# Optimization experiments

Measured on AMD Instinct MI355X. Metric: run time of the kernel, lower is better.

Reference implementation:

```python
import math
import jax, jax.numpy as jnp
import numpy as np

B, N, T, C, H = 16, 307, 24, 128, 8
D = C // H
FACTOR = 5
S = min(FACTOR * int(np.ceil(np.log(T))), T)   # sample_k (U_part) = 20
U = S                                          # n_top u = 20


def _pos_emb(t_len, c):
    pos = jnp.arange(t_len, dtype=jnp.float32)[:, None]
    div = jnp.exp(jnp.arange(0, c, 2, dtype=jnp.float32) * (-math.log(10000.0) / c))
    pe = jnp.zeros((t_len, c), dtype=jnp.float32)
    pe = pe.at[:, 0::2].set(jnp.sin(pos * div))
    pe = pe.at[:, 1::2].set(jnp.cos(pos * div))
    return pe  # [T, C]


def _layernorm(x, g, b, eps=1e-5):
    m = x.mean(-1, keepdims=True)
    v = ((x - m) ** 2).mean(-1, keepdims=True)
    return (x - m) / jnp.sqrt(v + eps) * g + b


def _forward(query, time_encoder, index_sample,
             emb_minute, emb_hour, emb_weekday, emb_month, emb_year,
             Wq, Wk, Wv, Wo, bo, ff_w1, ff_b1, ff_w2, ff_b2,
             ln1_g, ln1_b, ln2_g, ln2_b):
    # DataEmbedding: x + positional + temporal (dropout = identity in eval)
    pe = _pos_emb(T, C)                                   # [T, C]
    te = (emb_minute[time_encoder[..., 0]] + emb_hour[time_encoder[..., 1]]
          + emb_weekday[time_encoder[..., 2]] + emb_month[time_encoder[..., 3]]
          + emb_year[time_encoder[..., 4]])               # [B, T, C]
    x = query + pe[None, None, :, :] + te[:, None, :, :]  # [B, N, T, C]

    # QKV projections -> [B, H, N, T, D]
    def proj(inp, W):
        return (inp @ W).reshape(B, N, T, H, D).transpose(0, 3, 1, 2, 4)
    Q, K, V = proj(x, Wq), proj(x, Wk), proj(x, Wv)

    # ProbSparse: sample S keys per query position
    K_samp = K[:, :, :, index_sample, :]                  # [B, H, N, T, S, D]
    QK_samp = jnp.einsum('bhntd,bhntsd->bhnts', Q, K_samp)
    M = QK_samp.max(-1) - QK_samp.sum(-1) / S             # [B, H, N, T]
    _, M_top = jax.lax.top_k(M, U)                        # [B, H, N, U]

    Q_red = jnp.take_along_axis(Q, M_top[..., None], axis=3)  # [B, H, N, U, D]
    scores = jnp.einsum('bhnud,bhntd->bhnut', Q_red, K) * (1.0 / math.sqrt(D))
    attn = jax.nn.softmax(scores, axis=-1)
    upd = jnp.einsum('bhnut,bhntd->bhnud', attn, V)       # [B, H, N, U, D]

    # initial context = mean over T, then scatter-update top-u query rows
    ctx = jnp.broadcast_to(V.mean(axis=3, keepdims=True), V.shape)
    ctx = ctx.at[jnp.arange(B)[:, None, None, None],
                 jnp.arange(H)[None, :, None, None],
                 jnp.arange(N)[None, None, :, None],
                 M_top].set(upd)

    ctx = ctx.transpose(0, 2, 3, 1, 4).reshape(B, N, T, C)
    att_out = ctx @ Wo + bo

    x1 = _layernorm(att_out + x, ln1_g, ln1_b)
    ff = jax.nn.relu(x1 @ ff_w1 + ff_b1) @ ff_w2 + ff_b2
    out = _layernorm(ff + x1, ln2_g, ln2_b)
    return out


def setup_inputs() -> dict:
    key = jax.random.key(0)
    ks = jax.random.split(key, 32)
    def nrm(i, shape, s=0.02):
        return jax.random.normal(ks[i], shape, dtype=jnp.float32) * s
    inp = {
        'value': jax.random.normal(ks[0], (B, N, T, C), dtype=jnp.float32),
        'key_in': jax.random.normal(ks[1], (B, N, T, C), dtype=jnp.float32),
        'query': jax.random.normal(ks[2], (B, N, T, C), dtype=jnp.float32),
        't': 1,
        'time_encoder': jax.random.randint(ks[3], (B, T, 5), 0, 10),
        'index_sample': jax.random.randint(ks[4], (T, S), 0, T),
        'emb_minute': nrm(5, (70, C), 1.0), 'emb_hour': nrm(6, (30, C), 1.0),
        'emb_weekday': nrm(7, (10, C), 1.0), 'emb_month': nrm(8, (40, C), 1.0),
        'emb_year': nrm(9, (400, C), 1.0),
        'Wq': nrm(10, (C, C)), 'Wk': nrm(11, (C, C)), 'Wv': nrm(12, (C, C)),
        'Wo': nrm(13, (C, C)), 'bo': jnp.zeros((C,), jnp.float32),
        'ff_w1': nrm(14, (C, 4 * C)), 'ff_b1': jnp.zeros((4 * C,), jnp.float32),
        'ff_w2': nrm(15, (4 * C, C)), 'ff_b2': jnp.zeros((C,), jnp.float32),
        'ln1_g': jnp.ones((C,), jnp.float32), 'ln1_b': jnp.zeros((C,), jnp.float32),
        'ln2_g': jnp.ones((C,), jnp.float32), 'ln2_b': jnp.zeros((C,), jnp.float32),
    }
    return inp


def reference(value, key_in, query, t, time_encoder, index_sample,
              emb_minute, emb_hour, emb_weekday, emb_month, emb_year,
              Wq, Wk, Wv, Wo, bo, ff_w1, ff_b1, ff_w2, ff_b2,
              ln1_g, ln1_b, ln2_g, ln2_b):
    # value, key_in, t are accepted but unused, matching the torch module
    return _forward(query, time_encoder, index_sample,
                    emb_minute, emb_hour, emb_weekday, emb_month, emb_year,
                    Wq, Wk, Wv, Wo, bo, ff_w1, ff_b1, ff_w2, ff_b2,
                    ln1_g, ln1_b, ln2_g, ln2_b)
```

## Files before the change

### kernel.cpp

```cpp
#include <hip/hip_runtime.h>
#include <hip/hip_bf16.h>
#include <cmath>

namespace {
constexpr int B_ = 16, N_ = 307, T_ = 24, C_ = 128, H_ = 8, D_ = 16, S_ = 20, U_ = 20;
constexpr int NROW = B_ * N_ * T_;
constexpr int NX = NROW * C_;
constexpr int TEPE_N = B_ * T_ * C_;
constexpr int FF = 4 * C_;
constexpr int BM = 32;
constexpr int NBLK_MM = NROW / BM;
constexpr int BMT = 64;
constexpr int NBLK_T = NROW / BMT;
constexpr int NUNIT = B_ * H_ * N_;
}

typedef __attribute__((ext_vector_type(8))) short short8;
typedef __attribute__((ext_vector_type(4))) short short4_;
typedef __attribute__((ext_vector_type(4))) float f32x4;

__device__ inline short f2bf(float v) {
    union { float f; unsigned u; } a; a.f = v;
    unsigned r = a.u + 0x7fff + ((a.u >> 16) & 1);
    return (short)(r >> 16);
}
__device__ inline float bf2f(short s) {
    return __bfloat162float(*(const __hip_bfloat16*)&s);
}

__global__ void k_tepe(const int* __restrict__ te,
                       const float* __restrict__ e_min, const float* __restrict__ e_hr,
                       const float* __restrict__ e_wd, const float* __restrict__ e_mo,
                       const float* __restrict__ e_yr, float* __restrict__ tepe,
                       const int* __restrict__ idxs, unsigned char* __restrict__ cntg) {
    int i = blockIdx.x * blockDim.x + threadIdx.x;
    if (i < TEPE_N) {
        int c = i & (C_ - 1);
        int bt = i >> 7;
        int t = bt % T_;
        const int* enc = te + bt * 5;
        float v = e_min[enc[0] * C_ + c] + e_hr[enc[1] * C_ + c] + e_wd[enc[2] * C_ + c]
                + e_mo[enc[3] * C_ + c] + e_yr[enc[4] * C_ + c];
        float ang = (float)t * expf(-(float)(c & ~1) * (9.210340371976184f / 128.0f));
        v += (c & 1) ? cosf(ang) : sinf(ang);
        tepe[i] = v;
    }
    if (blockIdx.x == 0) {
        __shared__ int scnt[T_ * 32];
        for (int j = threadIdx.x; j < T_ * 32; j += 256) scnt[j] = 0;
        __syncthreads();
        for (int j = threadIdx.x; j < T_ * S_; j += 256) {
            int t = j / S_;
            atomicAdd(&scnt[t * 32 + idxs[j]], 1);
        }
        __syncthreads();
        for (int j = threadIdx.x; j < 192; j += 256) {
            unsigned v = (unsigned)scnt[4 * j] | ((unsigned)scnt[4 * j + 1] << 8)
                       | ((unsigned)scnt[4 * j + 2] << 16) | ((unsigned)scnt[4 * j + 3] << 24);
            ((unsigned*)cntg)[j] = v;
        }
    }
}

__global__ void k_wcvt_qkv(const float* __restrict__ Wq, const float* __restrict__ Wk,
                           const float* __restrict__ Wv, short* __restrict__ wqkvf) {
    int i = blockIdx.x * 256 + threadIdx.x;
    int tile = i >> 9, l = (i >> 3) & 63, e = i & 7;
    int c_tile = tile >> 2, ks = tile & 3;
    int c_all = c_tile * 16 + (l & 15);
    int k = ks * 32 + (l >> 4) * 8 + e;
    int m = c_all >> 7, c = c_all & (C_ - 1);
    const float* W = (m == 0) ? Wq : (m == 1) ? Wk : Wv;
    wqkvf[i] = f2bf(W[k * C_ + c]);
}

__global__ void k_wcvt2(const float* __restrict__ w1, const float* __restrict__ w2,
                        const float* __restrict__ Wo,
                        short* __restrict__ w1f, short* __restrict__ w2f,
                        short* __restrict__ wof) {
    int i = blockIdx.x * 256 + threadIdx.x;
    if (i < C_ * FF) {
        int tile = i >> 9, l = (i >> 3) & 63, e = i & 7;
        int jtile = tile >> 2, ks = tile & 3;
        int j = jtile * 16 + (l & 15);
        int k = ks * 32 + (l >> 4) * 8 + e;
        w1f[i] = f2bf(w1[k * FF + j]);
    } else if (i < 2 * C_ * FF) {
        int i2 = i - C_ * FF;
        int tile = i2 >> 9, l = (i2 >> 3) & 63, e = i2 & 7;
        int c_tile = tile >> 4, ks = tile & 15;
        int c = c_tile * 16 + (l & 15);
        int j = ks * 32 + (l >> 4) * 8 + e;
        w2f[i2] = f2bf(w2[j * C_ + c]);
    } else {
        int i3 = i - 2 * C_ * FF;
        int tile = i3 >> 9, l = (i3 >> 3) & 63, e = i3 & 7;
        int c_tile = tile >> 2, ks = tile & 3;
        int c = c_tile * 16 + (l & 15);
        int k = ks * 32 + (l >> 4) * 8 + e;
        wof[i3] = f2bf(Wo[k * C_ + c]);
    }
}

__global__ __launch_bounds__(256) void k_qkv_mfma(
    const float* __restrict__ query, const float* __restrict__ tepe,
    const short* __restrict__ wqkvf,
    short* __restrict__ Q, short* __restrict__ K, short* __restrict__ V) {
    __shared__ __align__(16) short xs[BM * C_];
    int tid = threadIdx.x;
    int r0 = blockIdx.x * BM;
    {
        int row = tid >> 3;
        int cb = (tid & 7) * 16;
        int gr = r0 + row;
        int t = gr % T_;
        int b = gr / (N_ * T_);
        const float* qsrc = query + (size_t)gr * C_ + cb;
        const float* tsrc = tepe + (size_t)(b * T_ + t) * C_ + cb;
        int swz0 = (row & 7) << 3;
#pragma unroll
        for (int i = 0; i < 4; i++) {
            float4 q4 = *(const float4*)(qsrc + 4 * i);
            float4 t4 = *(const float4*)(tsrc + 4 * i);
            short4_ sv;
            sv.x = f2bf(q4.x + t4.x); sv.y = f2bf(q4.y + t4.y);
            sv.z = f2bf(q4.z + t4.z); sv.w = f2bf(q4.w + t4.w);
            *(short4_*)&xs[(row * C_ + cb + 4 * i) ^ swz0] = sv;
        }
    }
    __syncthreads();
    int w = tid >> 6, l = tid & 63;
    int lr = l & 15, lk = l >> 4;
    int swz = (lr & 7) << 3;
    short8 bx[2][4];
#pragma unroll
    for (int rt = 0; rt < 2; rt++)
#pragma unroll
        for (int ks = 0; ks < 4; ks++)
            bx[rt][ks] = *(const short8*)&xs[((rt * 16 + lr) * C_ + ks * 32 + lk * 8) ^ swz];
    size_t base[2];
#pragma unroll
    for (int rt = 0; rt < 2; rt++) {
        int gr = r0 + rt * 16 + lr;
        int t = gr % T_;
        int n = (gr / T_) % N_;
        int b = gr / (N_ * T_);
        base[rt] = ((size_t)b * H_ * N_ + n) * (T_ * D_) + t * D_;
    }
#pragma unroll
    for (int jt = 0; jt < 6; jt++) {
        int ctile = w * 6 + jt;
        const short* ap = wqkvf + (size_t)ctile * 2048 + l * 8;
        short8 acur[4];
#pragma unroll
        for (int ks = 0; ks < 4; ks++) acur[ks] = *(const short8*)(ap + ks * 512);
        f32x4 acc[2] = {{0.f, 0.f, 0.f, 0.f}, {0.f, 0.f, 0.f, 0.f}};
#pragma unroll
        for (int ks = 0; ks < 4; ks++) {
#pragma unroll
            for (int rt = 0; rt < 2; rt++)
                acc[rt] = __builtin_amdgcn_mfma_f32_16x16x32_bf16(acur[ks], bx[rt][ks], acc[rt], 0, 0, 0);
        }
        int c0 = ctile * 16 + lk * 4;
        int m = c0 >> 7;
        int c = c0 & (C_ - 1);
        int h = c >> 4, d = c & 15;
        short* dst = (m == 0) ? Q : (m == 1) ? K : V;
#pragma unroll
        for (int rt = 0; rt < 2; rt++) {
            short4_ sv;
            sv.x = f2bf(acc[rt][0]); sv.y = f2bf(acc[rt][1]);
            sv.z = f2bf(acc[rt][2]); sv.w = f2bf(acc[rt][3]);
            *(short4_*)&dst[base[rt] + (size_t)h * (N_ * T_ * D_) + d] = sv;
        }
    }
}

__global__ __launch_bounds__(256) void k_attn(
    const short* __restrict__ Q, const short* __restrict__ K, const short* __restrict__ V,
    const unsigned char* __restrict__ cntg, short* __restrict__ ctx) {
    __shared__ __align__(16) short Qbf[4][32 * 24], Kbf[4][32 * 24];
    __shared__ __align__(16) short Vt[4][16 * 40];
    __shared__ __align__(16) short Pbf[4][32 * 40];
    __shared__ unsigned char cntS[T_ * 32];
    __shared__ float Mv[4][T_];
    __shared__ int keepS[4][T_];
    __shared__ float meanVs[4][D_];
    int tid = threadIdx.x;
    int wid = tid >> 6, l = tid & 63;
    int e = blockIdx.x * 4 + wid;
    const short* qb = Q + (size_t)e * (T_ * D_);
    const short* kb = K + (size_t)e * (T_ * D_);
    const short* vb = V + (size_t)e * (T_ * D_);
    if (l < 48) {
        int t = l >> 1, hf = l & 1;
        *(short8*)&Qbf[wid][t * 24 + hf * 8] = *(const short8*)(qb + t * 16 + hf * 8);
        *(short8*)&Kbf[wid][t * 24 + hf * 8] = *(const short8*)(kb + t * 16 + hf * 8);
    }
    for (int i = l; i < 96; i += 64) {
        int t = i >> 2, c4 = i & 3;
        short4_ v = *(const short4_*)(vb + t * 16 + c4 * 4);
        Vt[wid][(c4 * 4 + 0) * 40 + t] = v.x;
        Vt[wid][(c4 * 4 + 1) * 40 + t] = v.y;
        Vt[wid][(c4 * 4 + 2) * 40 + t] = v.z;
        Vt[wid][(c4 * 4 + 3) * 40 + t] = v.w;
    }
    for (int i = l; i < 128; i += 64) {
        int d = i >> 3, c = 24 + (i & 7);
        Vt[wid][d * 40 + c] = 0;
    }
    if (tid < 192) ((int*)cntS)[tid] = ((const int*)cntg)[tid];
    __syncthreads();
    if (l >= 48) {
        int d = l - 48;
        float s = 0.f;
        for (int t = 0; t < T_; t++) s += bf2f(Vt[wid][d * 40 + t]);
        meanVs[wid][d] = s * (1.0f / T_);
    }
    int lr = l & 15, lk = l >> 4;
    short8 zz = {};
    short8 kf0 = zz, kf1 = zz, qf0 = zz, qf1 = zz;
    if (lk < 2) {
        kf0 = *(const short8*)&Kbf[wid][lr * 24 + lk * 8];
        kf1 = *(const short8*)&Kbf[wid][(16 + lr) * 24 + lk * 8];
        qf0 = *(const short8*)&Qbf[wid][lr * 24 + lk * 8];
        qf1 = *(const short8*)&Qbf[wid][(16 + lr) * 24 + lk * 8];
    }
    f32x4 zf = {0.f, 0.f, 0.f, 0.f};
    f32x4 s00 = __builtin_amdgcn_mfma_f32_16x16x32_bf16(kf0, qf0, zf, 0, 0, 0);
    f32x4 s01 = __builtin_amdgcn_mfma_f32_16x16x32_bf16(kf1, qf0, zf, 0, 0, 0);
    f32x4 s10 = __builtin_amdgcn_mfma_f32_16x16x32_bf16(kf0, qf1, zf, 0, 0, 0);
    f32x4 s11 = __builtin_amdgcn_mfma_f32_16x16x32_bf16(kf1, qf1, zf, 0, 0, 0);
#pragma unroll
    for (int rt = 0; rt < 2; rt++) {
        int t = rt * 16 + lr;
        int tt = (t < T_) ? t : 0;
        f32x4 c0 = rt ? s10 : s00;
        f32x4 c1 = rt ? s11 : s01;
        float mx = -1e30f, sm = 0.f;
#pragma unroll
        for (int i = 0; i < 4; i++) {
            int cA = cntS[tt * 32 + lk * 4 + i];
            if (cA) { mx = fmaxf(mx, c0[i]); sm += (float)cA * c0[i]; }
        }
        if (lk < 2) {
#pragma unroll
            for (int i = 0; i < 4; i++) {
                int cB = cntS[tt * 32 + 16 + lk * 4 + i];
                if (cB) { mx = fmaxf(mx, c1[i]); sm += (float)cB * c1[i]; }
            }
        }
        mx = fmaxf(mx, __shfl_xor(mx, 16));
        mx = fmaxf(mx, __shfl_xor(mx, 32));
        sm += __shfl_xor(sm, 16);
        sm += __shfl_xor(sm, 32);
        if (lk == 0 && t < T_) Mv[wid][t] = mx - sm * (1.0f / S_);
    }
    __syncthreads();
    if (l < T_) {
        float mt = Mv[wid][l];
        int cnt2 = 0;
        for (int t2 = 0; t2 < T_; t2++) {
            float m2 = Mv[wid][t2];
            cnt2 += (m2 > mt) || (m2 == mt && t2 < l);
        }
        keepS[wid][l] = (cnt2 < U_) ? 1 : 0;
    }
#pragma unroll
    for (int rt = 0; rt < 2; rt++) {
        f32x4 c0 = rt ? s10 : s00;
        f32x4 c1 = rt ? s11 : s01;
        float lm = fmaxf(fmaxf(c0[0], c0[1]), fmaxf(c0[2], c0[3]));
        if (lk < 2) lm = fmaxf(lm, fmaxf(fmaxf(c1[0], c1[1]), fmaxf(c1[2], c1[3])));
        lm = fmaxf(lm, __shfl_xor(lm, 16));
        lm = fmaxf(lm, __shfl_xor(lm, 32));
        float e0[4], e1[4];
        float ls = 0.f;
#pragma unroll
        for (int i = 0; i < 4; i++) { e0[i] = __expf(0.25f * (c0[i] - lm)); ls += e0[i]; }
#pragma unroll
        for (int i = 0; i < 4; i++) { e1[i] = (lk < 2) ? __expf(0.25f * (c1[i] - lm)) : 0.f; ls += e1[i]; }
        ls += __shfl_xor(ls, 16);
        ls += __shfl_xor(ls, 32);
        float inv = 1.0f / ls;
        short4_ w0, w1;
        w0.x = f2bf(e0[0] * inv); w0.y = f2bf(e0[1] * inv);
        w0.z = f2bf(e0[2] * inv); w0.w = f2bf(e0[3] * inv);
        w1.x = f2bf(e1[0] * inv); w1.y = f2bf(e1[1] * inv);
        w1.z = f2bf(e1[2] * inv); w1.w = f2bf(e1[3] * inv);
        int trow = rt * 16 + lr;
        *(short4_*)&Pbf[wid][trow * 40 + lk * 4] = w0;
        *(short4_*)&Pbf[wid][trow * 40 + 16 + lk * 4] = w1;
    }
    __syncthreads();
    short8 vf = *(const short8*)&Vt[wid][lr * 40 + lk * 8];
    short8 pf0 = *(const short8*)&Pbf[wid][lr * 40 + lk * 8];
    short8 pf1 = *(const short8*)&Pbf[wid][(16 + lr) * 40 + lk * 8];
    f32x4 u0 = __builtin_amdgcn_mfma_f32_16x16x32_bf16(vf, pf0, zf, 0, 0, 0);
    f32x4 u1 = __builtin_amdgcn_mfma_f32_16x16x32_bf16(vf, pf1, zf, 0, 0, 0);
    int b = e / (H_ * N_);
    int h = (e / N_) % H_;
    int n = e % N_;
    float4 mv4 = *(const float4*)&meanVs[wid][lk * 4];
#pragma unroll
    for (int rt = 0; rt < 2; rt++) {
        int t = rt * 16 + lr;
        if (t < T_) {
            f32x4 u = rt ? u1 : u0;
            float4 o;
            if (keepS[wid][t]) { o.x = u[0]; o.y = u[1]; o.z = u[2]; o.w = u[3]; }
            else o = mv4;
            short4_ sv;
            sv.x = f2bf(o.x); sv.y = f2bf(o.y); sv.z = f2bf(o.z); sv.w = f2bf(o.w);
            *(short4_*)&ctx[((size_t)(b * N_ + n) * T_ + t) * C_ + h * D_ + lk * 4] = sv;
        }
    }
}

__global__ __launch_bounds__(256, 4) void k_tail(
    const short* __restrict__ ctx, const short* __restrict__ wof, const float* __restrict__ bo,
    const float* __restrict__ query, const float* __restrict__ tepe,
    const float* __restrict__ g1, const float* __restrict__ b1,
    const short* __restrict__ w1f, const float* __restrict__ b1f,
    const short* __restrict__ w2f, const float* __restrict__ b2f,
    const float* __restrict__ g2, const float* __restrict__ b2ln,
    float* __restrict__ out) {
    __shared__ __align__(16) char smem[81920];
    short* hbf = (short*)smem;
    float (*yf)[132] = (float(*)[132])smem;
    short* x1bf = (short*)(smem + 65536);
    int tid = threadIdx.x;
    int r0 = blockIdx.x * BMT;
    int w = tid >> 6, l = tid & 63;
    int lr = l & 15, lk = l >> 4;
    int swz = (lr & 7) << 3;
    int myloc = w * 16 + lr;
    int gr = r0 + myloc;
    int t = gr % T_;
    int b = gr / (N_ * T_);
    const short* csrc = ctx + (size_t)gr * C_;
    short8 bc[4];
#pragma unroll
    for (int ks = 0; ks < 4; ks++)
        bc[ks] = *(const short8*)(csrc + ks * 32 + lk * 8);
    const float* qsrc = query + (size_t)gr * C_;
    const float* tsrc = tepe + (size_t)(b * T_ + t) * C_;
    float4 xres[8];
#pragma unroll
    for (int ct = 0; ct < 8; ct++) {
        float4 q4 = *(const float4*)(qsrc + ct * 16 + lk * 4);
        float4 t4 = *(const float4*)(tsrc + ct * 16 + lk * 4);
        xres[ct].x = q4.x + t4.x; xres[ct].y = q4.y + t4.y;
        xres[ct].z = q4.z + t4.z; xres[ct].w = q4.w + t4.w;
    }
#pragma unroll
    for (int ct = 0; ct < 8; ct++) {
        f32x4 acc = {0.f, 0.f, 0.f, 0.f};
#pragma unroll
        for (int ks = 0; ks < 4; ks++) {
            short8 aw = *(const short8*)(wof + (size_t)(ct * 4 + ks) * 512 + l * 8);
            acc = __builtin_amdgcn_mfma_f32_16x16x32_bf16(aw, bc[ks], acc, 0, 0, 0);
        }
        float4 bo4 = *(const float4*)(bo + ct * 16 + lk * 4);
        xres[ct].x += acc[0] + bo4.x;
        xres[ct].y += acc[1] + bo4.y;
        xres[ct].z += acc[2] + bo4.z;
        xres[ct].w += acc[3] + bo4.w;
    }
    {
        float s = 0.f;
#pragma unroll
        for (int ct = 0; ct < 8; ct++)
            s += xres[ct].x + xres[ct].y + xres[ct].z + xres[ct].w;
        s += __shfl_xor(s, 16);
        s += __shfl_xor(s, 32);
        float mean = s * (1.f / C_);
        float vv = 0.f;
#pragma unroll
        for (int ct = 0; ct < 8; ct++) {
            float dx = xres[ct].x - mean, dy = xres[ct].y - mean;
            float dz = xres[ct].z - mean, dw = xres[ct].w - mean;
            vv += dx * dx + dy * dy + dz * dz + dw * dw;
        }
        vv += __shfl_xor(vv, 16);
        vv += __shfl_xor(vv, 32);
        float rstd = rsqrtf(vv * (1.f / C_) + 1e-5f);
#pragma unroll
        for (int ct = 0; ct < 8; ct++) {
            float4 gv = *(const float4*)(g1 + ct * 16 + lk * 4);
            float4 bv = *(const float4*)(b1 + ct * 16 + lk * 4);
            short4_ xv;
            xv.x = f2bf((xres[ct].x - mean) * rstd * gv.x + bv.x);
            xv.y = f2bf((xres[ct].y - mean) * rstd * gv.y + bv.y);
            xv.z = f2bf((xres[ct].z - mean) * rstd * gv.z + bv.z);
            xv.w = f2bf((xres[ct].w - mean) * rstd * gv.w + bv.w);
            *(short4_*)&x1bf[(myloc * C_ + ct * 16 + lk * 4) ^ swz] = xv;
        }
    }
    const short* w1base = w1f + (size_t)(w * 8) * 2048 + l * 8;
    short8 acur[4];
#pragma unroll
    for (int ks = 0; ks < 4; ks++) acur[ks] = *(const short8*)(w1base + ks * 512);
    __syncthreads();
    {
        short8 bx[4][4];
#pragma unroll
        for (int rt = 0; rt < 4; rt++)
#pragma unroll
            for (int ks = 0; ks < 4; ks++)
                bx[rt][ks] = *(const short8*)&x1bf[((rt * 16 + lr) * C_ + ks * 32 + lk * 8) ^ swz];
#pragma unroll
        for (int jt = 0; jt < 8; jt++) {
            short8 anxt[4];
            if (jt < 7) {
#pragma unroll
                for (int ks = 0; ks < 4; ks++)
                    anxt[ks] = *(const short8*)(w1base + (size_t)(jt + 1) * 2048 + ks * 512);
            }
            f32x4 a1[4] = {{0.f, 0.f, 0.f, 0.f}, {0.f, 0.f, 0.f, 0.f},
                           {0.f, 0.f, 0.f, 0.f}, {0.f, 0.f, 0.f, 0.f}};
#pragma unroll
            for (int ks = 0; ks < 4; ks++) {
#pragma unroll
                for (int rt = 0; rt < 4; rt++)
                    a1[rt] = __builtin_amdgcn_mfma_f32_16x16x32_bf16(acur[ks], bx[rt][ks], a1[rt], 0, 0, 0);
            }
            int j0 = (w * 8 + jt) * 16 + lk * 4;
            float4 b1v = *(const float4*)(b1f + j0);
#pragma unroll
            for (int rt = 0; rt < 4; rt++) {
                int rr = rt * 16 + lr;
                short4_ hv;
                hv.x = f2bf(fmaxf(a1[rt][0] + b1v.x, 0.f));
                hv.y = f2bf(fmaxf(a1[rt][1] + b1v.y, 0.f));
                hv.z = f2bf(fmaxf(a1[rt][2] + b1v.z, 0.f));
                hv.w = f2bf(fmaxf(a1[rt][3] + b1v.w, 0.f));
                *(short4_*)&hbf[(rr * FF + j0) ^ swz] = hv;
            }
#pragma unroll
            for (int ks = 0; ks < 4; ks++) acur[ks] = anxt[ks];
        }
    }
    short8 aA[2];
#pragma unroll
    for (int ct = 0; ct < 2; ct++)
        aA[ct] = *(const short8*)(w2f + (size_t)((w * 2 + ct) * 16) * 512 + l * 8);
    __syncthreads();
    f32x4 acc2[2][4] = {{{0.f, 0.f, 0.f, 0.f}, {0.f, 0.f, 0.f, 0.f},
                         {0.f, 0.f, 0.f, 0.f}, {0.f, 0.f, 0.f, 0.f}},
                        {{0.f, 0.f, 0.f, 0.f}, {0.f, 0.f, 0.f, 0.f},
                         {0.f, 0.f, 0.f, 0.f}, {0.f, 0.f, 0.f, 0.f}}};
#pragma unroll 4
    for (int ks = 0; ks < 16; ks++) {
        short8 aB[2];
        if (ks < 15) {
#pragma unroll
            for (int ct = 0; ct < 2; ct++)
                aB[ct] = *(const short8*)(w2f + (size_t)((w * 2 + ct) * 16 + ks + 1) * 512 + l * 8);
        }
        short8 hx[4];
#pragma unroll
        for (int rt = 0; rt < 4; rt++)
            hx[rt] = *(const short8*)&hbf[((rt * 16 + lr) * FF + ks * 32 + lk * 8) ^ swz];
#pragma unroll
        for (int ct = 0; ct < 2; ct++)
#pragma unroll
            for (int rt = 0; rt < 4; rt++)
                acc2[ct][rt] = __builtin_amdgcn_mfma_f32_16x16x32_bf16(aA[ct], hx[rt], acc2[ct][rt], 0, 0, 0);
#pragma unroll
        for (int ct = 0; ct < 2; ct++) aA[ct] = aB[ct];
    }
    float4 res[2][4], b2v[2];
#pragma unroll
    for (int ct = 0; ct < 2; ct++) {
        int cc = (w * 2 + ct) * 16 + lk * 4;
        b2v[ct] = *(const float4*)(b2f + cc);
#pragma unroll
        for (int rt = 0; rt < 4; rt++) {
            short4_ rb = *(const short4_*)&x1bf[((rt * 16 + lr) * C_ + cc) ^ swz];
            res[ct][rt].x = bf2f(rb.x); res[ct][rt].y = bf2f(rb.y);
            res[ct][rt].z = bf2f(rb.z); res[ct][rt].w = bf2f(rb.w);
        }
    }
    __syncthreads();
#pragma unroll
    for (int ct = 0; ct < 2; ct++) {
        int cc = (w * 2 + ct) * 16 + lk * 4;
#pragma unroll
        for (int rt = 0; rt < 4; rt++) {
            int rr = rt * 16 + lr;
            float4 o;
            o.x = acc2[ct][rt][0] + b2v[ct].x + res[ct][rt].x;
            o.y = acc2[ct][rt][1] + b2v[ct].y + res[ct][rt].y;
            o.z = acc2[ct][rt][2] + b2v[ct].z + res[ct][rt].z;
            o.w = acc2[ct][rt][3] + b2v[ct].w + res[ct][rt].w;
            *(float4*)&yf[rr][cc] = o;
        }
    }
    __syncthreads();
#pragma unroll
    for (int half = 0; half < 2; half++) {
        int r = (tid >> 3) + half * 32;
        int q = tid & 7;
        int cb = q * 16;
        float vals[16];
        float s = 0.f;
#pragma unroll
        for (int i = 0; i < 16; i++) { vals[i] = yf[r][cb + i]; s += vals[i]; }
        s += __shfl_xor(s, 1, 8);
        s += __shfl_xor(s, 2, 8);
        s += __shfl_xor(s, 4, 8);
        float mean = s * (1.f / C_);
        float vv = 0.f;
#pragma unroll
        for (int i = 0; i < 16; i++) { float d = vals[i] - mean; vv += d * d; }
        vv += __shfl_xor(vv, 1, 8);
        vv += __shfl_xor(vv, 2, 8);
        vv += __shfl_xor(vv, 4, 8);
        float rstd = rsqrtf(vv * (1.f / C_) + 1e-5f);
        float* op = out + (size_t)(r0 + r) * C_ + cb;
#pragma unroll
        for (int i4 = 0; i4 < 4; i4++) {
            float4 gv = *(const float4*)(g2 + cb + 4 * i4);
            float4 bv = *(const float4*)(b2ln + cb + 4 * i4);
            float4 ov;
            ov.x = (vals[4 * i4 + 0] - mean) * rstd * gv.x + bv.x;
            ov.y = (vals[4 * i4 + 1] - mean) * rstd * gv.y + bv.y;
            ov.z = (vals[4 * i4 + 2] - mean) * rstd * gv.z + bv.z;
            ov.w = (vals[4 * i4 + 3] - mean) * rstd * gv.w + bv.w;
            *(float4*)(op + 4 * i4) = ov;
        }
    }
}

extern "C" void kernel_launch(void* const* d_in, const int* in_sizes, int n_in,
                              void* d_out, int out_size, void* d_ws, size_t ws_size,
                              hipStream_t stream) {
    const float* query = (const float*)d_in[2];
    const int* time_enc = (const int*)d_in[4];
    const int* index_sample = (const int*)d_in[5];
    const float* e_min = (const float*)d_in[6];
    const float* e_hr  = (const float*)d_in[7];
    const float* e_wd  = (const float*)d_in[8];
    const float* e_mo  = (const float*)d_in[9];
    const float* e_yr  = (const float*)d_in[10];
    const float* Wq = (const float*)d_in[11];
    const float* Wk = (const float*)d_in[12];
    const float* Wv = (const float*)d_in[13];
    const float* Wo = (const float*)d_in[14];
    const float* bo = (const float*)d_in[15];
    const float* ffw1 = (const float*)d_in[16];
    const float* ffb1 = (const float*)d_in[17];
    const float* ffw2 = (const float*)d_in[18];
    const float* ffb2 = (const float*)d_in[19];
    const float* ln1g = (const float*)d_in[20];
    const float* ln1b = (const float*)d_in[21];
    const float* ln2g = (const float*)d_in[22];
    const float* ln2b = (const float*)d_in[23];

    float* ws = (float*)d_ws;
    float* tepe = ws;
    float* region1 = ws + TEPE_N;
    float* region2 = region1 + NX;
    float* region3 = region2 + NX;
    float* region4 = region3 + NX;

    short* Qb = (short*)region1;
    short* Kb = (short*)region2;
    short* Vb = (short*)region3;
    short* ctxb = (short*)region4;
    short* wqkvf = (short*)region4 + NX;
    unsigned char* cntg = (unsigned char*)((short*)region4 + NX + 49152);
    short* w1f = (short*)region2;
    short* w2f = w1f + C_ * FF;
    short* wof = w2f + C_ * FF;

    k_tepe<<<dim3(TEPE_N / 256), dim3(256), 0, stream>>>(
        time_enc, e_min, e_hr, e_wd, e_mo, e_yr, tepe, index_sample, cntg);
    k_wcvt_qkv<<<dim3(384 * C_ / 256), dim3(256), 0, stream>>>(Wq, Wk, Wv, wqkvf);
    k_qkv_mfma<<<dim3(NBLK_MM), dim3(256), 0, stream>>>(
        query, tepe, wqkvf, Qb, Kb, Vb);
    k_attn<<<dim3(NUNIT / 4), dim3(256), 0, stream>>>(
        Qb, Kb, Vb, cntg, ctxb);
    k_wcvt2<<<dim3((2 * C_ * FF + C_ * C_) / 256), dim3(256), 0, stream>>>(
        ffw1, ffw2, Wo, w1f, w2f, wof);
    k_tail<<<dim3(NBLK_T), dim3(256), 0, stream>>>(
        ctxb, wof, bo, query, tepe, ln1g, ln1b,
        w1f, ffb1, w2f, ffb2, ln2g, ln2b, (float*)d_out);
}
```

Before: 174.0 us.

## Merge prep kernels, drop block barriers in attention, chunk FFN hidden to cut LDS

Folds the embedding/pos-enc, QKV weight conversion and FFN/Wo weight conversion into one prep kernel, removing two launches. The weight buffers move to just past the K region so they can be written before attention runs. In the attention kernel, block-wide barriers are dropped because each wave works only on its own LDS slices, relying on wave-level ordering. The tail FFN processes the 512-wide hidden layer in two 256-wide chunks, shrinking LDS from 80KB to 48KB for higher occupancy, at the cost of extra barriers and reloading x1 fragments from LDS.

```diff
diff --git a/kernel.cpp b/kernel.cpp
--- a/kernel.cpp
+++ b/kernel.cpp
@@ -13,6 +13,7 @@
 constexpr int BMT = 64;
 constexpr int NBLK_T = NROW / BMT;
 constexpr int NUNIT = B_ * H_ * N_;
+constexpr int PREP_N = TEPE_N + 384 * C_ + (2 * C_ * FF + C_ * C_);
 }
 
 typedef __attribute__((ext_vector_type(8))) short short8;
@@ -28,12 +29,18 @@
     return __bfloat162float(*(const __hip_bfloat16*)&s);
 }
 
-__global__ void k_tepe(const int* __restrict__ te,
+__global__ void k_prep(const int* __restrict__ te,
                        const float* __restrict__ e_min, const float* __restrict__ e_hr,
                        const float* __restrict__ e_wd, const float* __restrict__ e_mo,
                        const float* __restrict__ e_yr, float* __restrict__ tepe,
-                       const int* __restrict__ idxs, unsigned char* __restrict__ cntg) {
-    int i = blockIdx.x * blockDim.x + threadIdx.x;
+                       const int* __restrict__ idxs, unsigned char* __restrict__ cntg,
+                       const float* __restrict__ Wq, const float* __restrict__ Wk,
+                       const float* __restrict__ Wv, short* __restrict__ wqkvf,
+                       const float* __restrict__ w1, const float* __restrict__ w2,
+                       const float* __restrict__ Wo,
+                       short* __restrict__ w1f, short* __restrict__ w2f,
+                       short* __restrict__ wof) {
+    int i = blockIdx.x * 256 + threadIdx.x;
     if (i < TEPE_N) {
         int c = i & (C_ - 1);
         int bt = i >> 7;
@@ -44,6 +51,38 @@
         float ang = (float)t * expf(-(float)(c & ~1) * (9.210340371976184f / 128.0f));
         v += (c & 1) ? cosf(ang) : sinf(ang);
         tepe[i] = v;
+    } else if (i < TEPE_N + 384 * C_) {
+        int j = i - TEPE_N;
+        int tile = j >> 9, l = (j >> 3) & 63, e = j & 7;
+        int c_tile = tile >> 2, ks = tile & 3;
+        int c_all = c_tile * 16 + (l & 15);
+        int k = ks * 32 + (l >> 4) * 8 + e;
+        int m = c_all >> 7, c = c_all & (C_ - 1);
+        const float* W = (m == 0) ? Wq : (m == 1) ? Wk : Wv;
+        wqkvf[j] = f2bf(W[k * C_ + c]);
+    } else {
+        int j = i - TEPE_N - 384 * C_;
+        if (j < C_ * FF) {
+            int tile = j >> 9, l = (j >> 3) & 63, e = j & 7;
+            int jtile = tile >> 2, ks = tile & 3;
+            int jj = jtile * 16 + (l & 15);
+            int k = ks * 32 + (l >> 4) * 8 + e;
+            w1f[j] = f2bf(w1[k * FF + jj]);
+        } else if (j < 2 * C_ * FF) {
+            int j2 = j - C_ * FF;
+            int tile = j2 >> 9, l = (j2 >> 3) & 63, e = j2 & 7;
+            int c_tile = tile >> 4, ks = tile & 15;
+            int c = c_tile * 16 + (l & 15);
+            int jj = ks * 32 + (l >> 4) * 8 + e;
+            w2f[j2] = f2bf(w2[jj * C_ + c]);
+        } else {
+            int j3 = j - 2 * C_ * FF;
+            int tile = j3 >> 9, l = (j3 >> 3) & 63, e = j3 & 7;
+            int c_tile = tile >> 2, ks = tile & 3;
+            int c = c_tile * 16 + (l & 15);
+            int k = ks * 32 + (l >> 4) * 8 + e;
+            wof[j3] = f2bf(Wo[k * C_ + c]);
+        }
     }
     if (blockIdx.x == 0) {
         __shared__ int scnt[T_ * 32];
@@ -59,46 +98,6 @@
                        | ((unsigned)scnt[4 * j + 2] << 16) | ((unsigned)scnt[4 * j + 3] << 24);
             ((unsigned*)cntg)[j] = v;
         }
-    }
-}
-
-__global__ void k_wcvt_qkv(const float* __restrict__ Wq, const float* __restrict__ Wk,
-                           const float* __restrict__ Wv, short* __restrict__ wqkvf) {
-    int i = blockIdx.x * 256 + threadIdx.x;
-    int tile = i >> 9, l = (i >> 3) & 63, e = i & 7;
-    int c_tile = tile >> 2, ks = tile & 3;
-    int c_all = c_tile * 16 + (l & 15);
-    int k = ks * 32 + (l >> 4) * 8 + e;
-    int m = c_all >> 7, c = c_all & (C_ - 1);
-    const float* W = (m == 0) ? Wq : (m == 1) ? Wk : Wv;
-    wqkvf[i] = f2bf(W[k * C_ + c]);
-}
-
-__global__ void k_wcvt2(const float* __restrict__ w1, const float* __restrict__ w2,
-                        const float* __restrict__ Wo,
-                        short* __restrict__ w1f, short* __restrict__ w2f,
-                        short* __restrict__ wof) {
-    int i = blockIdx.x * 256 + threadIdx.x;
-    if (i < C_ * FF) {
-        int tile = i >> 9, l = (i >> 3) & 63, e = i & 7;
-        int jtile = tile >> 2, ks = tile & 3;
-        int j = jtile * 16 + (l & 15);
-        int k = ks * 32 + (l >> 4) * 8 + e;
-        w1f[i] = f2bf(w1[k * FF + j]);
-    } else if (i < 2 * C_ * FF) {
-        int i2 = i - C_ * FF;
-        int tile = i2 >> 9, l = (i2 >> 3) & 63, e = i2 & 7;
-        int c_tile = tile >> 4, ks = tile & 15;
-        int c = c_tile * 16 + (l & 15);
-        int j = ks * 32 + (l >> 4) * 8 + e;
-        w2f[i2] = f2bf(w2[j * C_ + c]);
-    } else {
-        int i3 = i - 2 * C_ * FF;
-        int tile = i3 >> 9, l = (i3 >> 3) & 63, e = i3 & 7;
-        int c_tile = tile >> 2, ks = tile & 3;
-        int c = c_tile * 16 + (l & 15);
-        int k = ks * 32 + (l >> 4) * 8 + e;
-        wof[i3] = f2bf(Wo[k * C_ + c]);
     }
 }
 
@@ -209,8 +208,8 @@
         int d = i >> 3, c = 24 + (i & 7);
         Vt[wid][d * 40 + c] = 0;
     }
-    if (tid < 192) ((int*)cntS)[tid] = ((const int*)cntg)[tid];
-    __syncthreads();
+    for (int i = l; i < 192; i += 64)
+        ((int*)cntS)[i] = ((const int*)cntg)[i];
     if (l >= 48) {
         int d = l - 48;
         float s = 0.f;
@@ -256,7 +255,6 @@
         sm += __shfl_xor(sm, 32);
         if (lk == 0 && t < T_) Mv[wid][t] = mx - sm * (1.0f / S_);
     }
-    __syncthreads();
     if (l < T_) {
         float mt = Mv[wid][l];
         int cnt2 = 0;
@@ -292,7 +290,6 @@
         *(short4_*)&Pbf[wid][trow * 40 + lk * 4] = w0;
         *(short4_*)&Pbf[wid][trow * 40 + 16 + lk * 4] = w1;
     }
-    __syncthreads();
     short8 vf = *(const short8*)&Vt[wid][lr * 40 + lk * 8];
     short8 pf0 = *(const short8*)&Pbf[wid][lr * 40 + lk * 8];
     short8 pf1 = *(const short8*)&Pbf[wid][(16 + lr) * 40 + lk * 8];
@@ -325,10 +322,10 @@
     const short* __restrict__ w2f, const float* __restrict__ b2f,
     const float* __restrict__ g2, const float* __restrict__ b2ln,
     float* __restrict__ out) {
-    __shared__ __align__(16) char smem[81920];
+    __shared__ __align__(16) char smem[49152];
     short* hbf = (short*)smem;
     float (*yf)[132] = (float(*)[132])smem;
-    short* x1bf = (short*)(smem + 65536);
+    short* x1bf = (short*)(smem + 32768);
     int tid = threadIdx.x;
     int r0 = blockIdx.x * BMT;
     int w = tid >> 6, l = tid & 63;
@@ -397,36 +394,44 @@
             *(short4_*)&x1bf[(myloc * C_ + ct * 16 + lk * 4) ^ swz] = xv;
         }
     }
-    const short* w1base = w1f + (size_t)(w * 8) * 2048 + l * 8;
-    short8 acur[4];
-#pragma unroll
-    for (int ks = 0; ks < 4; ks++) acur[ks] = *(const short8*)(w1base + ks * 512);
+    short8 pre1[4];
+    {
+        const short* ap = w1f + (size_t)(w * 4) * 2048 + l * 8;
+#pragma unroll
+        for (int ks = 0; ks < 4; ks++) pre1[ks] = *(const short8*)(ap + ks * 512);
+    }
     __syncthreads();
-    {
-        short8 bx[4][4];
-#pragma unroll
-        for (int rt = 0; rt < 4; rt++)
-#pragma unroll
-            for (int ks = 0; ks < 4; ks++)
-                bx[rt][ks] = *(const short8*)&x1bf[((rt * 16 + lr) * C_ + ks * 32 + lk * 8) ^ swz];
-#pragma unroll
-        for (int jt = 0; jt < 8; jt++) {
-            short8 anxt[4];
-            if (jt < 7) {
-#pragma unroll
-                for (int ks = 0; ks < 4; ks++)
-                    anxt[ks] = *(const short8*)(w1base + (size_t)(jt + 1) * 2048 + ks * 512);
+    f32x4 acc2[2][4] = {{{0.f, 0.f, 0.f, 0.f}, {0.f, 0.f, 0.f, 0.f},
+                         {0.f, 0.f, 0.f, 0.f}, {0.f, 0.f, 0.f, 0.f}},
+                        {{0.f, 0.f, 0.f, 0.f}, {0.f, 0.f, 0.f, 0.f},
+                         {0.f, 0.f, 0.f, 0.f}, {0.f, 0.f, 0.f, 0.f}}};
+    for (int p = 0; p < 2; p++) {
+        for (int jt = 0; jt < 4; jt++) {
+            int jtile = p * 16 + w * 4 + jt;
+            short8 acur[4];
+            if (p == 0 && jt == 0) {
+#pragma unroll
+                for (int ks = 0; ks < 4; ks++) acur[ks] = pre1[ks];
+            } else {
+                const short* ap = w1f + (size_t)jtile * 2048 + l * 8;
+#pragma unroll
+                for (int ks = 0; ks < 4; ks++) acur[ks] = *(const short8*)(ap + ks * 512);
             }
             f32x4 a1[4] = {{0.f, 0.f, 0.f, 0.f}, {0.f, 0.f, 0.f, 0.f},
                            {0.f, 0.f, 0.f, 0.f}, {0.f, 0.f, 0.f, 0.f}};
 #pragma unroll
             for (int ks = 0; ks < 4; ks++) {
+                short8 bx4[4];
 #pragma unroll
                 for (int rt = 0; rt < 4; rt++)
-                    a1[rt] = __builtin_amdgcn_mfma_f32_16x16x32_bf16(acur[ks], bx[rt][ks], a1[rt], 0, 0, 0);
+                    bx4[rt] = *(const short8*)&x1bf[((rt * 16 + lr) * C_ + ks * 32 + lk * 8) ^ swz];
+#pragma unroll
+                for (int rt = 0; rt < 4; rt++)
+                    a1[rt] = __builtin_amdgcn_mfma_f32_16x16x32_bf16(acur[ks], bx4[rt], a1[rt], 0, 0, 0);
             }
-            int j0 = (w * 8 + jt) * 16 + lk * 4;
-            float4 b1v = *(const float4*)(b1f + j0);
+            int j0g = jtile * 16 + lk * 4;
+            int j0l = (w * 4 + jt) * 16 + lk * 4;
+            float4 b1v = *(const float4*)(b1f + j0g);
 #pragma unroll
             for (int rt = 0; rt < 4; rt++) {
                 int rr = rt * 16 + lr;
@@ -435,40 +440,25 @@
                 hv.y = f2bf(fmaxf(a1[rt][1] + b1v.y, 0.f));
                 hv.z = f2bf(fmaxf(a1[rt][2] + b1v.z, 0.f));
                 hv.w = f2bf(fmaxf(a1[rt][3] + b1v.w, 0.f));
-                *(short4_*)&hbf[(rr * FF + j0) ^ swz] = hv;
+                *(short4_*)&hbf[(rr * 256 + j0l) ^ swz] = hv;
             }
-#pragma unroll
-            for (int ks = 0; ks < 4; ks++) acur[ks] = anxt[ks];
-        }
-    }
-    short8 aA[2];
-#pragma unroll
-    for (int ct = 0; ct < 2; ct++)
-        aA[ct] = *(const short8*)(w2f + (size_t)((w * 2 + ct) * 16) * 512 + l * 8);
-    __syncthreads();
-    f32x4 acc2[2][4] = {{{0.f, 0.f, 0.f, 0.f}, {0.f, 0.f, 0.f, 0.f},
-                         {0.f, 0.f, 0.f, 0.f}, {0.f, 0.f, 0.f, 0.f}},
-                        {{0.f, 0.f, 0.f, 0.f}, {0.f, 0.f, 0.f, 0.f},
-                         {0.f, 0.f, 0.f, 0.f}, {0.f, 0.f, 0.f, 0.f}}};
-#pragma unroll 4
-    for (int ks = 0; ks < 16; ks++) {
-        short8 aB[2];
-        if (ks < 15) {
-#pragma unroll
-            for (int ct = 0; ct < 2; ct++)
-                aB[ct] = *(const short8*)(w2f + (size_t)((w * 2 + ct) * 16 + ks + 1) * 512 + l * 8);
-        }
-        short8 hx[4];
-#pragma unroll
-        for (int rt = 0; rt < 4; rt++)
-            hx[rt] = *(const short8*)&hbf[((rt * 16 + lr) * FF + ks * 32 + lk * 8) ^ swz];
-#pragma unroll
-        for (int ct = 0; ct < 2; ct++)
+        }
+        __syncthreads();
+#pragma unroll 2
+        for (int ks = 0; ks < 8; ks++) {
+            short8 hx[4];
 #pragma unroll
             for (int rt = 0; rt < 4; rt++)
-                acc2[ct][rt] = __builtin_amdgcn_mfma_f32_16x16x32_bf16(aA[ct], hx[rt], acc2[ct][rt], 0, 0, 0);
-#pragma unroll
-        for (int ct = 0; ct < 2; ct++) aA[ct] = aB[ct];
+                hx[rt] = *(const short8*)&hbf[((rt * 16 + lr) * 256 + ks * 32 + lk * 8) ^ swz];
+#pragma unroll
+            for (int ct = 0; ct < 2; ct++) {
+                short8 aw = *(const short8*)(w2f + ((size_t)((w * 2 + ct) * 16 + p * 8 + ks)) * 512 + l * 8);
+#pragma unroll
+                for (int rt = 0; rt < 4; rt++)
+                    acc2[ct][rt] = __builtin_amdgcn_mfma_f32_16x16x32_bf16(aw, hx[rt], acc2[ct][rt], 0, 0, 0);
+            }
+        }
+        __syncthreads();
     }
     float4 res[2][4], b2v[2];
 #pragma unroll
@@ -571,19 +561,17 @@
     short* ctxb = (short*)region4;
     short* wqkvf = (short*)region4 + NX;
     unsigned char* cntg = (unsigned char*)((short*)region4 + NX + 49152);
-    short* w1f = (short*)region2;
+    short* w1f = (short*)region2 + NX;
     short* w2f = w1f + C_ * FF;
     short* wof = w2f + C_ * FF;
 
-    k_tepe<<<dim3(TEPE_N / 256), dim3(256), 0, stream>>>(
-        time_enc, e_min, e_hr, e_wd, e_mo, e_yr, tepe, index_sample, cntg);
-    k_wcvt_qkv<<<dim3(384 * C_ / 256), dim3(256), 0, stream>>>(Wq, Wk, Wv, wqkvf);
+    k_prep<<<dim3(PREP_N / 256), dim3(256), 0, stream>>>(
+        time_enc, e_min, e_hr, e_wd, e_mo, e_yr, tepe, index_sample, cntg,
+        Wq, Wk, Wv, wqkvf, ffw1, ffw2, Wo, w1f, w2f, wof);
     k_qkv_mfma<<<dim3(NBLK_MM), dim3(256), 0, stream>>>(
         query, tepe, wqkvf, Qb, Kb, Vb);
     k_attn<<<dim3(NUNIT / 4), dim3(256), 0, stream>>>(
         Qb, Kb, Vb, cntg, ctxb);
-    k_wcvt2<<<dim3((2 * C_ * FF + C_ * C_) / 256), dim3(256), 0, stream>>>(
-        ffw1, ffw2, Wo, w1f, w2f, wof);
     k_tail<<<dim3(NBLK_T), dim3(256), 0, stream>>>(
         ctxb, wof, bo, query, tepe, ln1g, ln1b,
         w1f, ffb1, w2f, ffb2, ln2g, ln2b, (float*)d_out);
```

Result: slower. 185.8 us (+6.8%).
